# Optimization experiments

Hardware: AMD Instinct MI355X
Metric: run time of the kernel (lower is better)

The kernel has to match this reference:

```python
import jax, jax.numpy as jnp
import numpy as np

N_NODES = 40000
N_EDGES = 640000
D_IN = 128
D_HID = 128
D_OUT = 128


def _glorot(key, shape):
    fan_in, fan_out = shape[1], shape[0]
    lim = np.sqrt(6.0 / (fan_in + fan_out))
    return jax.random.uniform(key, shape, jnp.float32, -lim, lim)


def setup_inputs() -> dict:
    key = jax.random.key(0)
    ks = jax.random.split(key, 8)
    x = jax.random.normal(ks[0], (N_NODES, D_IN), jnp.float32)
    edge_index = jax.random.randint(ks[1], (2, N_EDGES), 0, N_NODES, jnp.int64)
    return {
        "x": x,
        "edge_index": edge_index,
        # layer 1 (SAGEConv -> hidden): lin_l (neighbor branch, with bias), lin_r (root, no bias)
        "W1_l": _glorot(ks[2], (D_HID, D_IN)),
        "b1_l": jnp.zeros((D_HID,), jnp.float32),
        "W1_r": _glorot(ks[3], (D_HID, D_IN)),
        # layer 2 (SAGEConv -> out)
        "W2_l": _glorot(ks[4], (D_OUT, D_HID)),
        "b2_l": jnp.zeros((D_OUT,), jnp.float32),
        "W2_r": _glorot(ks[5], (D_OUT, D_HID)),
    }


def _sage_conv(x, src, dst, W_l, b_l, W_r, n_nodes):
    # mean aggregation of source features at destination nodes
    msg_sum = jax.ops.segment_sum(x[src], dst, num_segments=n_nodes)  # [N, D]
    deg = jax.ops.segment_sum(jnp.ones((src.shape[0],), x.dtype), dst,
                              num_segments=n_nodes)  # [N]
    mean = msg_sum / jnp.maximum(deg, 1.0)[:, None]  # zero for isolated nodes
    return mean @ W_l.T + b_l + x @ W_r.T


def reference(x, edge_index, W1_l, b1_l, W1_r, W2_l, b2_l, W2_r):
    src, dst = edge_index[0], edge_index[1]
    n = x.shape[0]
    h = _sage_conv(x, src, dst, W1_l, b1_l, W1_r, n)
    h = jax.nn.relu(h)
    out = _sage_conv(h, src, dst, W2_l, b2_l, W2_r, n)
    return out
```

## Files before the change

kernel.cpp:

```cpp
#include <hip/hip_runtime.h>

#define N_NODES 40000
#define N_EDGES 640000
#define D 128
#define ELLW 48
#define SENT 40000

typedef __attribute__((ext_vector_type(8))) short short8;
typedef __attribute__((ext_vector_type(4))) float f32x4;
typedef __attribute__((ext_vector_type(2))) float f32x2;

__device__ __forceinline__ unsigned short f2bf(float f) {
  unsigned int u = __float_as_uint(f);
  u += 0x7fffu + ((u >> 16) & 1u);
  return (unsigned short)(u >> 16);
}
__device__ __forceinline__ float bflo(unsigned int v) { return __uint_as_float(v << 16); }
__device__ __forceinline__ float bfhi(unsigned int v) { return __uint_as_float(v & 0xffff0000u); }

__device__ __forceinline__ unsigned int pk_fp8x4(float a, float b, float c, float d) {
  int v = __builtin_amdgcn_cvt_pk_fp8_f32(a, b, 0, false);
  v = __builtin_amdgcn_cvt_pk_fp8_f32(c, d, v, true);
  return (unsigned int)v;
}
__device__ __forceinline__ void acc_fp8x4(unsigned int u, float* a) {
  f32x2 p0 = __builtin_amdgcn_cvt_pk_f32_fp8(u, false);
  f32x2 p1 = __builtin_amdgcn_cvt_pk_f32_fp8(u, true);
  a[0] += p0[0]; a[1] += p0[1]; a[2] += p1[0]; a[3] += p1[1];
}

__global__ void k_prep(const float* __restrict__ x, unsigned short* __restrict__ xb,
                       unsigned short* __restrict__ hb,
                       unsigned char* __restrict__ xf8, unsigned char* __restrict__ hf8,
                       int* __restrict__ deg, unsigned short* __restrict__ ell,
                       const float* __restrict__ w0, const float* __restrict__ w1,
                       const float* __restrict__ w2, const float* __restrict__ w3,
                       unsigned short* __restrict__ o0, unsigned short* __restrict__ o1,
                       unsigned short* __restrict__ o2, unsigned short* __restrict__ o3) {
  int b = blockIdx.x;
  int tid = threadIdx.x;
  if (b < 5000) {
    int i = b * 256 + tid;
    if (i < N_NODES / 4) ((int4*)deg)[i] = make_int4(0, 0, 0, 0);
    float4 v = ((const float4*)x)[i];
    unsigned int lo = (unsigned int)f2bf(v.x) | ((unsigned int)f2bf(v.y) << 16);
    unsigned int hi = (unsigned int)f2bf(v.z) | ((unsigned int)f2bf(v.w) << 16);
    ((uint2*)xb)[i] = make_uint2(lo, hi);
    ((unsigned int*)xf8)[i] = pk_fp8x4(v.x, v.y, v.z, v.w);
  } else if (b < 5064) {
    if (b == 5000) {
      if (tid < 64) {
        ((unsigned int*)(xb + (size_t)SENT * D))[tid] = 0u;
        ((unsigned int*)(hb + (size_t)SENT * D))[tid] = 0u;
      } else if (tid < 96) {
        ((unsigned int*)(xf8 + (size_t)SENT * D))[tid - 64] = 0u;
      } else if (tid < 128) {
        ((unsigned int*)(hf8 + (size_t)SENT * D))[tid - 96] = 0u;
      }
    }
    int i = (b - 5000) * 256 + tid;
    int m = i >> 12, j = i & 4095;
    const float* s = (m == 0) ? w0 : (m == 1) ? w1 : (m == 2) ? w2 : w3;
    unsigned short* o = (m == 0) ? o0 : (m == 1) ? o1 : (m == 2) ? o2 : o3;
    float4 v = ((const float4*)s)[j];
    unsigned int lo = (unsigned int)f2bf(v.x) | ((unsigned int)f2bf(v.y) << 16);
    unsigned int hi = (unsigned int)f2bf(v.z) | ((unsigned int)f2bf(v.w) << 16);
    ((uint2*)o)[j] = make_uint2(lo, hi);
  } else {
    int i = (b - 5064) * 256 + tid;
    if (i < N_NODES * ELLW / 8) {
      unsigned int sv = (SENT & 0xffffu) | ((unsigned int)SENT << 16);
      uint4 q; q.x = sv; q.y = sv; q.z = sv; q.w = sv;
      ((uint4*)ell)[i] = q;
    }
  }
}

__global__ void k_fillell(const int* __restrict__ src, const int* __restrict__ dst,
                          int* __restrict__ deg, unsigned short* __restrict__ ell) {
  int e = blockIdx.x * 256 + threadIdx.x;
  if (e < N_EDGES) {
    int d = dst[e];
    int pos = atomicAdd(&deg[d], 1);
    if (pos < ELLW) ell[(size_t)d * ELLW + pos] = (unsigned short)src[e];
  }
}

__global__ void k_agg(const uint4* __restrict__ t8, const int* __restrict__ deg,
                      const unsigned short* __restrict__ ell, uint4* __restrict__ mean4) {
  int node = blockIdx.x * 4 + (threadIdx.x >> 6);
  int lane = threadIdx.x & 63;
  int g = lane >> 3;
  int s = lane & 7;
  int d = deg[node];
  int cnt = d < ELLW ? d : ELLW;
  int cntp = (cnt + 15) & ~15;
  const unsigned short* row = ell + (size_t)node * ELLW;
  float a[16];
#pragma unroll
  for (int i = 0; i < 16; ++i) a[i] = 0.f;
  for (int e = 0; e < cntp; e += 16) {
    int sA = row[e + g];
    int sB = row[e + 8 + g];
    uint4 vA = t8[(size_t)sA * 8 + s];
    uint4 vB = t8[(size_t)sB * 8 + s];
    acc_fp8x4(vA.x, a + 0); acc_fp8x4(vA.y, a + 4);
    acc_fp8x4(vA.z, a + 8); acc_fp8x4(vA.w, a + 12);
    acc_fp8x4(vB.x, a + 0); acc_fp8x4(vB.y, a + 4);
    acc_fp8x4(vB.z, a + 8); acc_fp8x4(vB.w, a + 12);
  }
#pragma unroll
  for (int st = 8; st <= 32; st <<= 1) {
#pragma unroll
    for (int i = 0; i < 16; ++i) a[i] += __shfl_xor(a[i], st);
  }
  if (g == 0) {
    float inv = 1.0f / (float)(d > 1 ? d : 1);
#pragma unroll
    for (int i = 0; i < 16; ++i) a[i] *= inv;
    uint4 o0, o1;
    o0.x = (unsigned int)f2bf(a[0]) | ((unsigned int)f2bf(a[1]) << 16);
    o0.y = (unsigned int)f2bf(a[2]) | ((unsigned int)f2bf(a[3]) << 16);
    o0.z = (unsigned int)f2bf(a[4]) | ((unsigned int)f2bf(a[5]) << 16);
    o0.w = (unsigned int)f2bf(a[6]) | ((unsigned int)f2bf(a[7]) << 16);
    o1.x = (unsigned int)f2bf(a[8]) | ((unsigned int)f2bf(a[9]) << 16);
    o1.y = (unsigned int)f2bf(a[10]) | ((unsigned int)f2bf(a[11]) << 16);
    o1.z = (unsigned int)f2bf(a[12]) | ((unsigned int)f2bf(a[13]) << 16);
    o1.w = (unsigned int)f2bf(a[14]) | ((unsigned int)f2bf(a[15]) << 16);
    mean4[(size_t)node * 16 + s * 2] = o0;
    mean4[(size_t)node * 16 + s * 2 + 1] = o1;
  }
}

__global__ __launch_bounds__(64) void k_gemm(
    const unsigned short* __restrict__ Al, const unsigned short* __restrict__ Ar,
    const unsigned short* __restrict__ Wl, const unsigned short* __restrict__ Wr,
    const float* __restrict__ bias,
    unsigned short* __restrict__ out_bf, unsigned char* __restrict__ out_f8,
    float* __restrict__ out_f, int relu_bf16) {
  const int lane = threadIdx.x;
  const int m0 = blockIdx.x * 32;
  const int ml = lane & 15;
  const int kg = lane >> 4;
  const unsigned short* al0 = Al + (size_t)(m0 + ml) * 128 + kg * 8;
  const unsigned short* ar0 = Ar + (size_t)(m0 + ml) * 128 + kg * 8;
  const unsigned short* al1 = al0 + 16 * 128;
  const unsigned short* ar1 = ar0 + 16 * 128;
  const unsigned short* wl_p = Wl + (size_t)ml * 128 + kg * 8;
  const unsigned short* wr_p = Wr + (size_t)ml * 128 + kg * 8;

  f32x4 acc[2][8];
#pragma unroll
  for (int mt = 0; mt < 2; ++mt)
#pragma unroll
    for (int nt = 0; nt < 8; ++nt) acc[mt][nt] = 0;

#pragma unroll
  for (int kt = 0; kt < 4; ++kt) {
    short8 a0l = *(const short8*)(al0 + kt * 32);
    short8 a0r = *(const short8*)(ar0 + kt * 32);
    short8 a1l = *(const short8*)(al1 + kt * 32);
    short8 a1r = *(const short8*)(ar1 + kt * 32);
#pragma unroll
    for (int nt = 0; nt < 8; ++nt) {
      short8 b_l = *(const short8*)(wl_p + nt * 2048 + kt * 32);
      short8 b_r = *(const short8*)(wr_p + nt * 2048 + kt * 32);
      acc[0][nt] = __builtin_amdgcn_mfma_f32_16x16x32_bf16(a0l, b_l, acc[0][nt], 0, 0, 0);
      acc[0][nt] = __builtin_amdgcn_mfma_f32_16x16x32_bf16(a0r, b_r, acc[0][nt], 0, 0, 0);
      acc[1][nt] = __builtin_amdgcn_mfma_f32_16x16x32_bf16(a1l, b_l, acc[1][nt], 0, 0, 0);
      acc[1][nt] = __builtin_amdgcn_mfma_f32_16x16x32_bf16(a1r, b_r, acc[1][nt], 0, 0, 0);
    }
  }

#pragma unroll
  for (int mt = 0; mt < 2; ++mt) {
    const int orow = m0 + mt * 16 + kg * 4;
#pragma unroll
    for (int nt = 0; nt < 8; ++nt) {
      int col = nt * 16 + ml;
      float b = bias[col];
#pragma unroll
      for (int r = 0; r < 4; ++r) {
        float o = acc[mt][nt][r] + b;
        if (relu_bf16) {
          o = fmaxf(o, 0.f);
          out_bf[(size_t)(orow + r) * 128 + col] = f2bf(o);
          unsigned int p8 = (unsigned int)__builtin_amdgcn_cvt_pk_fp8_f32(o, o, 0, false);
          out_f8[(size_t)(orow + r) * 128 + col] = (unsigned char)(p8 & 0xffu);
        } else {
          out_f[(size_t)(orow + r) * 128 + col] = o;
        }
      }
    }
  }
}

extern "C" void kernel_launch(void* const* d_in, const int* in_sizes, int n_in,
                              void* d_out, int out_size, void* d_ws, size_t ws_size,
                              hipStream_t stream) {
  const float* x   = (const float*)d_in[0];
  const int*   ei  = (const int*)d_in[1];
  const float* W1l = (const float*)d_in[2];
  const float* b1l = (const float*)d_in[3];
  const float* W1r = (const float*)d_in[4];
  const float* W2l = (const float*)d_in[5];
  const float* b2l = (const float*)d_in[6];
  const float* W2r = (const float*)d_in[7];
  const int* srcp = ei;
  const int* dstp = ei + N_EDGES;

  char* ws = (char*)d_ws;
  size_t off = 0;
  auto alloc = [&](size_t bytes) {
    void* p = ws + off;
    off = (off + bytes + 255) & ~(size_t)255;
    return p;
  };
  int* deg             = (int*)alloc((size_t)N_NODES * 4);
  unsigned short* ell  = (unsigned short*)alloc((size_t)N_NODES * ELLW * 2);
  unsigned short* w1lb = (unsigned short*)alloc((size_t)D * D * 2);
  unsigned short* w1rb = (unsigned short*)alloc((size_t)D * D * 2);
  unsigned short* w2lb = (unsigned short*)alloc((size_t)D * D * 2);
  unsigned short* w2rb = (unsigned short*)alloc((size_t)D * D * 2);
  unsigned short* xb   = (unsigned short*)alloc((size_t)(N_NODES + 1) * D * 2);
  unsigned short* mb   = (unsigned short*)alloc((size_t)N_NODES * D * 2);
  unsigned short* hb   = (unsigned short*)alloc((size_t)(N_NODES + 1) * D * 2);
  unsigned char* xf8   = (unsigned char*)alloc((size_t)(N_NODES + 1) * D);
  unsigned char* hf8   = (unsigned char*)alloc((size_t)(N_NODES + 1) * D);

  k_prep<<<6002, 256, 0, stream>>>(x, xb, hb, xf8, hf8, deg, ell,
                                   W1l, W1r, W2l, W2r, w1lb, w1rb, w2lb, w2rb);

  k_fillell<<<(N_EDGES + 255) / 256, 256, 0, stream>>>(srcp, dstp, deg, ell);

  k_agg<<<N_NODES / 4, 256, 0, stream>>>((const uint4*)xf8, deg, ell, (uint4*)mb);
  k_gemm<<<N_NODES / 32, 64, 0, stream>>>(mb, xb, w1lb, w1rb, b1l, hb, hf8, nullptr, 1);

  k_agg<<<N_NODES / 4, 256, 0, stream>>>((const uint4*)hf8, deg, ell, (uint4*)mb);
  k_gemm<<<N_NODES / 32, 64, 0, stream>>>(mb, hb, w2lb, w2rb, b2l, nullptr, nullptr,
                                          (float*)d_out, 0);
}
```

Before: 127.2 us.

## Assign one node per 8 lanes in aggregation instead of one per wavefront

The aggregation kernel now maps each destination node to 8 lanes, one per 16-byte feature chunk. It walks the node's neighbor list sequentially, four at a time, instead of spreading neighbors across 8 lane groups and reducing them with cross-lane shuffles. Padding drops from multiples of 16 to multiples of 4, so fewer sentinel rows are gathered, and the shuffle reduction and idle-store lanes are gone. In exchange each lane does a longer serial loop, and lanes in a wavefront diverge when node degrees differ.

```diff
diff --git a/kernel.cpp b/kernel.cpp
--- a/kernel.cpp
+++ b/kernel.cpp
@@ -88,48 +88,44 @@
 
 __global__ void k_agg(const uint4* __restrict__ t8, const int* __restrict__ deg,
                       const unsigned short* __restrict__ ell, uint4* __restrict__ mean4) {
-  int node = blockIdx.x * 4 + (threadIdx.x >> 6);
-  int lane = threadIdx.x & 63;
-  int g = lane >> 3;
-  int s = lane & 7;
+  int node = blockIdx.x * 32 + (threadIdx.x >> 3);
+  int s = threadIdx.x & 7;
   int d = deg[node];
   int cnt = d < ELLW ? d : ELLW;
-  int cntp = (cnt + 15) & ~15;
+  int cntp = (cnt + 3) & ~3;
   const unsigned short* row = ell + (size_t)node * ELLW;
   float a[16];
 #pragma unroll
   for (int i = 0; i < 16; ++i) a[i] = 0.f;
-  for (int e = 0; e < cntp; e += 16) {
-    int sA = row[e + g];
-    int sB = row[e + 8 + g];
-    uint4 vA = t8[(size_t)sA * 8 + s];
-    uint4 vB = t8[(size_t)sB * 8 + s];
-    acc_fp8x4(vA.x, a + 0); acc_fp8x4(vA.y, a + 4);
-    acc_fp8x4(vA.z, a + 8); acc_fp8x4(vA.w, a + 12);
-    acc_fp8x4(vB.x, a + 0); acc_fp8x4(vB.y, a + 4);
-    acc_fp8x4(vB.z, a + 8); acc_fp8x4(vB.w, a + 12);
-  }
-#pragma unroll
-  for (int st = 8; st <= 32; st <<= 1) {
-#pragma unroll
-    for (int i = 0; i < 16; ++i) a[i] += __shfl_xor(a[i], st);
-  }
-  if (g == 0) {
-    float inv = 1.0f / (float)(d > 1 ? d : 1);
-#pragma unroll
-    for (int i = 0; i < 16; ++i) a[i] *= inv;
-    uint4 o0, o1;
-    o0.x = (unsigned int)f2bf(a[0]) | ((unsigned int)f2bf(a[1]) << 16);
-    o0.y = (unsigned int)f2bf(a[2]) | ((unsigned int)f2bf(a[3]) << 16);
-    o0.z = (unsigned int)f2bf(a[4]) | ((unsigned int)f2bf(a[5]) << 16);
-    o0.w = (unsigned int)f2bf(a[6]) | ((unsigned int)f2bf(a[7]) << 16);
-    o1.x = (unsigned int)f2bf(a[8]) | ((unsigned int)f2bf(a[9]) << 16);
-    o1.y = (unsigned int)f2bf(a[10]) | ((unsigned int)f2bf(a[11]) << 16);
-    o1.z = (unsigned int)f2bf(a[12]) | ((unsigned int)f2bf(a[13]) << 16);
-    o1.w = (unsigned int)f2bf(a[14]) | ((unsigned int)f2bf(a[15]) << 16);
-    mean4[(size_t)node * 16 + s * 2] = o0;
-    mean4[(size_t)node * 16 + s * 2 + 1] = o1;
-  }
+  for (int e = 0; e < cntp; e += 4) {
+    int i0 = row[e], i1 = row[e + 1], i2 = row[e + 2], i3 = row[e + 3];
+    uint4 v0 = t8[(size_t)i0 * 8 + s];
+    uint4 v1 = t8[(size_t)i1 * 8 + s];
+    uint4 v2 = t8[(size_t)i2 * 8 + s];
+    uint4 v3 = t8[(size_t)i3 * 8 + s];
+    acc_fp8x4(v0.x, a + 0); acc_fp8x4(v0.y, a + 4);
+    acc_fp8x4(v0.z, a + 8); acc_fp8x4(v0.w, a + 12);
+    acc_fp8x4(v1.x, a + 0); acc_fp8x4(v1.y, a + 4);
+    acc_fp8x4(v1.z, a + 8); acc_fp8x4(v1.w, a + 12);
+    acc_fp8x4(v2.x, a + 0); acc_fp8x4(v2.y, a + 4);
+    acc_fp8x4(v2.z, a + 8); acc_fp8x4(v2.w, a + 12);
+    acc_fp8x4(v3.x, a + 0); acc_fp8x4(v3.y, a + 4);
+    acc_fp8x4(v3.z, a + 8); acc_fp8x4(v3.w, a + 12);
+  }
+  float inv = 1.0f / (float)(d > 1 ? d : 1);
+#pragma unroll
+  for (int i = 0; i < 16; ++i) a[i] *= inv;
+  uint4 o0, o1;
+  o0.x = (unsigned int)f2bf(a[0]) | ((unsigned int)f2bf(a[1]) << 16);
+  o0.y = (unsigned int)f2bf(a[2]) | ((unsigned int)f2bf(a[3]) << 16);
+  o0.z = (unsigned int)f2bf(a[4]) | ((unsigned int)f2bf(a[5]) << 16);
+  o0.w = (unsigned int)f2bf(a[6]) | ((unsigned int)f2bf(a[7]) << 16);
+  o1.x = (unsigned int)f2bf(a[8]) | ((unsigned int)f2bf(a[9]) << 16);
+  o1.y = (unsigned int)f2bf(a[10]) | ((unsigned int)f2bf(a[11]) << 16);
+  o1.z = (unsigned int)f2bf(a[12]) | ((unsigned int)f2bf(a[13]) << 16);
+  o1.w = (unsigned int)f2bf(a[14]) | ((unsigned int)f2bf(a[15]) << 16);
+  mean4[(size_t)node * 16 + s * 2] = o0;
+  mean4[(size_t)node * 16 + s * 2 + 1] = o1;
 }
 
 __global__ __launch_bounds__(64) void k_gemm(
@@ -233,10 +229,10 @@
 
   k_fillell<<<(N_EDGES + 255) / 256, 256, 0, stream>>>(srcp, dstp, deg, ell);
 
-  k_agg<<<N_NODES / 4, 256, 0, stream>>>((const uint4*)xf8, deg, ell, (uint4*)mb);
+  k_agg<<<N_NODES / 32, 256, 0, stream>>>((const uint4*)xf8, deg, ell, (uint4*)mb);
   k_gemm<<<N_NODES / 32, 64, 0, stream>>>(mb, xb, w1lb, w1rb, b1l, hb, hf8, nullptr, 1);
 
-  k_agg<<<N_NODES / 4, 256, 0, stream>>>((const uint4*)hf8, deg, ell, (uint4*)mb);
+  k_agg<<<N_NODES / 32, 256, 0, stream>>>((const uint4*)hf8, deg, ell, (uint4*)mb);
   k_gemm<<<N_NODES / 32, 64, 0, stream>>>(mb, hb, w2lb, w2rb, b2l, nullptr, nullptr,
                                           (float*)d_out, 0);
 }
```

New measurement: 106.1 us, median of 2. 1.2x faster.
